# Kernel tuning notes

Measured on AMD Instinct MI355X. Metric: run time of the kernel, lower is better.

The kernel has to match this reference:

```python
import jax, jax.numpy as jnp
import numpy as np

N_CLASS, N_SUPPORT, N_QUERY = 5, 5, 15
C, T, V = 128, 8, 25
LN_EPS = 1e-12


def setup_inputs() -> dict:
    key = jax.random.key(0)
    ks = jax.random.split(key, 6)
    n_tot = N_CLASS * (N_SUPPORT + N_QUERY)
    inp = jax.random.normal(ks[0], (n_tot, C, T, V), dtype=jnp.float32)
    # episode labels: 20 consecutive samples per class (arange // per_class)
    target = (jnp.arange(n_tot, dtype=jnp.int32) // (N_SUPPORT + N_QUERY)).astype(jnp.int32)
    s = 0.02
    p = lambda k: jax.random.normal(k, (C, C), dtype=jnp.float32) * s
    return {
        'input': inp,
        'Wq': p(ks[1]), 'bq': jnp.zeros((C,), jnp.float32),
        'Wk': p(ks[2]), 'bk': jnp.zeros((C,), jnp.float32),
        'Wv': p(ks[3]), 'bv': jnp.zeros((C,), jnp.float32),
        'Wo': p(ks[4]), 'bo': jnp.zeros((C,), jnp.float32),
        'ln_g': jnp.ones((C,), jnp.float32), 'ln_b': jnp.zeros((C,), jnp.float32),
        'target': target,
        'n_support': N_SUPPORT,
    }


def _layer_norm(x, g, b):
    mu = x.mean(-1, keepdims=True)
    var = ((x - mu) ** 2).mean(-1, keepdims=True)
    return (x - mu) * jax.lax.rsqrt(var + LN_EPS) * g + b


def _episode_forward(input, Wq, bq, Wk, bk, Wv, bv, Wo, bo, ln_g, ln_b, target, n_support):
    n_tot, c, t, v = input.shape
    m = N_CLASS
    per_class = n_tot // m
    n_query = per_class - n_support
    n = m * n_query

    # support/query split (stable argsort == torch.where per class for sorted labels)
    order = jnp.argsort(target).reshape(m, per_class)
    supp_idx = order[:, :n_support]                      # (m, h)
    qry_idx = order[:, n_support:].reshape(-1)           # (n,)
    z_proto = input[supp_idx]                            # (m, h, c, t, v)
    zq = input[qry_idx]                                  # (n, c, t, v)

    # ---- hal(): pairwise cross-attention over the vertex axis ----
    mh = m * n_support
    zq_p = jnp.transpose(zq, (0, 2, 3, 1))                                   # (n, t, v, c)
    zp_p = jnp.transpose(z_proto.reshape(mh, c, t, v), (0, 2, 3, 1))          # (mh, t, v, c)
    cat = jnp.concatenate([zq_p, zp_p], axis=0)                               # (n1, t, v, c)
    n1 = cat.shape[0]

    # Q from each of the n1 items, K/V from each of the mh prototypes.
    # Equivalent to the original expand->reshape pairing, without duplicating K/V.
    Q = cat @ Wq + bq                                                         # (n1, t, v, c)
    K = zp_p @ Wk + bk                                                        # (mh, t, v, c)
    Vv = zp_p @ Wv + bv                                                       # (mh, t, v, c)
    scale = 1.0 / jnp.sqrt(jnp.asarray(c, dtype=Q.dtype))
    scores = jnp.einsum('ntqc,mtkc->nmtqk', Q, K) * scale                     # (n1, mh, t, v, v)
    attn = jax.nn.softmax(scores, axis=-1)
    ctx = jnp.einsum('nmtqk,mtkc->nmtqc', attn, Vv)                           # (n1, mh, t, v, c)
    out = _layer_norm(ctx @ Wo + bo + cat[:, None], ln_g, ln_b)               # residual + LN
    att = out.mean(axis=1)                                                    # (n1, t, v, c) mean over mh pairs

    zq_att = jnp.transpose(att[:n], (0, 3, 1, 2))                             # (n, c, t, v)
    proto_att = att[n:].reshape(m, n_support, t, v, c).mean(axis=1)           # (m, t, v, c)
    proto_att = jnp.transpose(proto_att, (0, 3, 1, 2))                        # (m, c, t, v)

    # ---- squared-Euclidean metric on flattened features ----
    zq_f = zq_att.reshape(n, -1)
    zp_f = proto_att.reshape(m, -1)
    dist = jnp.sum((zq_f[:, None, :] - zp_f[None, :, :]) ** 2, axis=-1)       # (n, m)

    log_p_y = jax.nn.log_softmax(-dist, axis=1).reshape(m, n_query, m)
    cls = jnp.arange(m)
    loss = -log_p_y[cls[:, None], jnp.arange(n_query)[None, :], cls[:, None]].mean()
    y_hat = jnp.argmax(log_p_y, axis=2)
    acc = (y_hat == cls[:, None]).astype(jnp.float32).mean()
    return loss, acc


def reference(input, Wq, bq, Wk, bk, Wv, bv, Wo, bo, ln_g, ln_b, target, n_support):
    return _episode_forward(input, Wq, bq, Wk, bk, Wv, bv, Wo, bo, ln_g, ln_b, target, n_support)
```

## Files before the change

kernel.cpp:

```cpp
#include <hip/hip_runtime.h>
#include <math.h>

#define NTOT 100
#define NQ   75
#define NP   25
#define CC   128
#define TT   8
#define VV   25
#define NCLS 5
#define NSUP 5
#define NQRY 15
#define ROW  (TT*VV*CC)
#define TILE (VV*CC)
#define ROWS_Q 20000
#define ROWS_S 5000
#define RB_Q 625
#define RB_S 157

typedef __attribute__((ext_vector_type(8))) short short8;
typedef __attribute__((ext_vector_type(16))) float f32x16;

typedef union { uint4 u4; short8 s8; } pk_t;

__device__ __forceinline__ ushort f2bf(float f) {
    uint u = __float_as_uint(f);
    u += 0x7FFFu + ((u >> 16) & 1u);
    return (ushort)(u >> 16);
}
__device__ __forceinline__ float bf2f(uint u16v) {
    return __uint_as_float(u16v << 16);
}
__device__ __forceinline__ uint pkbf(float a, float b) {
    return (uint)f2bf(a) | ((uint)f2bf(b) << 16);
}

__global__ __launch_bounds__(256) void k_pack(
    const float* __restrict__ Wq, const float* __restrict__ Wk,
    const float* __restrict__ Wv, const float* __restrict__ Wo,
    ushort* __restrict__ WfG) {
    int which = blockIdx.x;
    const float* W = (which == 0) ? Wq : (which == 1) ? Wk : (which == 2) ? Wv : Wo;
    ushort* dstbase = WfG + (size_t)which * 16384;
    for (int o = threadIdx.x; o < 2048; o += 256) {
        int k8 = o >> 7, c = o & 127;
        uint4 pk;
        pk.x = pkbf(W[(k8*8+0)*128 + c], W[(k8*8+1)*128 + c]);
        pk.y = pkbf(W[(k8*8+2)*128 + c], W[(k8*8+3)*128 + c]);
        pk.z = pkbf(W[(k8*8+4)*128 + c], W[(k8*8+5)*128 + c]);
        pk.w = pkbf(W[(k8*8+6)*128 + c], W[(k8*8+7)*128 + c]);
        int dst = (((c >> 5) * 8 + (k8 >> 1)) * 64 + ((c & 31) + 32 * (k8 & 1))) * 8;
        *(uint4*)(dstbase + dst) = pk;
    }
}

__global__ __launch_bounds__(256) void k_proj(
    const float* __restrict__ input, const int* __restrict__ target,
    const ushort* __restrict__ WfG,
    const float* __restrict__ bq, const float* __restrict__ bk,
    const float* __restrict__ bv,
    ushort* __restrict__ catC, ushort* __restrict__ Qf,
    ushort* __restrict__ Kf, ushort* __restrict__ Vf,
    int* __restrict__ counter) {
    __shared__ ushort stage[32 * 132];
    __shared__ ushort VtF[4096];
    __shared__ int iscr[200];

    int bid = blockIdx.x, tid = threadIdx.x;
    int w = tid >> 6, lane = tid & 63, half = lane >> 5, l31 = lane & 31;

    if (bid == 0 && tid == 0) *counter = 0;

    if (tid < NTOT) iscr[tid] = target[tid];
    __syncthreads();
    if (tid < NTOT) {
        int ti = iscr[tid], rank = 0;
        for (int j = 0; j < NTOT; ++j) {
            int tj = iscr[j];
            rank += (tj < ti) || (tj == ti && j < tid);
        }
        iscr[100 + rank] = tid;
    }
    __syncthreads();

    bool isQ = bid >= RB_S;
    int rowblk = isQ ? bid - RB_S : bid;
    int rlimit = isQ ? ROWS_Q : ROWS_S;
    int g0 = rowblk * 32;
    int gend = min(g0 + 32, rlimit);

    for (int nn = g0 / 200; nn <= (gend - 1) / 200; ++nn) {
        int lo = max(g0 - nn * 200, 0);
        int hi = min(gend - 1 - nn * 200, 199);
        int len = hi - lo + 1;
        int nidx = isQ ? nn : (NQ + nn);
        int src;
        if (nidx < NQ) { int m = nidx / NQRY, qq = nidx - m * NQRY; src = iscr[100 + m * 20 + NSUP + qq]; }
        else           { int i2 = nidx - NQ; int m = i2 / NSUP, s = i2 - m * NSUP; src = iscr[100 + m * 20 + s]; }
        const float* inb = input + (size_t)src * ROW + lo;
        int rbase = nn * 200 + lo - g0;
        for (int idx = tid; idx < len * 128; idx += 256) {
            int c = idx / len, k = idx - c * len;
            stage[(rbase + k) * 132 + c] = f2bf(inb[c * 200 + k]);
        }
    }
    __syncthreads();

    short8 af[8];
    #pragma unroll
    for (int ks = 0; ks < 8; ++ks)
        af[ks] = *(const short8*)&stage[l31 * 132 + ks * 16 + half * 8];

    #define CHAIN(A, OUT, BASE) do {                                             \
        const ushort* bp_ = (BASE) + w * 4096 + lane * 8;                        \
        _Pragma("unroll")                                                        \
        for (int ks = 0; ks < 8; ++ks) {                                         \
            short8 bf_ = *(const short8*)(bp_ + ks * 512);                       \
            OUT = __builtin_amdgcn_mfma_f32_32x32x16_bf16(A[ks], bf_, OUT, 0, 0, 0); \
        }                                                                        \
    } while (0)

    if (isQ) {
        f32x16 Cm;
        #pragma unroll
        for (int r = 0; r < 16; ++r) Cm[r] = 0.f;
        CHAIN(af, Cm, WfG);
        float bcol = bq[w * 32 + l31];
        int c = w * 32 + l31;
        #pragma unroll
        for (int r = 0; r < 16; ++r) {
            int row = g0 + (r & 3) + 8 * (r >> 2) + 4 * half;
            int st = row / 25, vv = row - st * 25;
            size_t dst = (((size_t)st * 8 + (c >> 4)) * 64 + (vv + 32 * ((c >> 3) & 1))) * 8 + (c & 7);
            Qf[dst] = f2bf(Cm[r] + bcol);
        }
        uint* cc = (uint*)catC + (size_t)g0 * 64;
        for (int idx = tid; idx < 2048; idx += 256) {
            int row = idx >> 6, c2 = (idx & 63) * 2;
            cc[idx] = (uint)stage[row * 132 + c2] | ((uint)stage[row * 132 + c2 + 1] << 16);
        }
    } else {
        {
            f32x16 Cm;
            #pragma unroll
            for (int r = 0; r < 16; ++r) Cm[r] = 0.f;
            CHAIN(af, Cm, WfG + 16384);
            float bcol = bk[w * 32 + l31];
            int c = w * 32 + l31;
            #pragma unroll
            for (int r = 0; r < 16; ++r) {
                int row = g0 + (r & 3) + 8 * (r >> 2) + 4 * half;
                if (row < ROWS_S) {
                    int st = row / 25, vv = row - st * 25;
                    size_t dst = (((size_t)st * 8 + (c >> 4)) * 64 + (vv + 32 * ((c >> 3) & 1))) * 8 + (c & 7);
                    Kf[dst] = f2bf(Cm[r] + bcol);
                }
            }
        }
        {
            f32x16 Cm;
            #pragma unroll
            for (int r = 0; r < 16; ++r) Cm[r] = 0.f;
            CHAIN(af, Cm, WfG + 32768);
            float bcol = bv[w * 32 + l31];
            int c = w * 32 + l31;
            int ks2 = c >> 4, kh = (c >> 3) & 1, j2 = c & 7;
            #pragma unroll
            for (int r = 0; r < 16; ++r) {
                int rowLocal = (r & 3) + 8 * (r >> 2) + 4 * half;
                VtF[ks2 * 512 + (rowLocal + 32 * kh) * 8 + j2] = f2bf(Cm[r] + bcol);
            }
        }
        __syncthreads();
        short8 a2[8];
        #pragma unroll
        for (int ks = 0; ks < 8; ++ks)
            a2[ks] = *(const short8*)&VtF[ks * 512 + lane * 8];
        {
            f32x16 Cm;
            #pragma unroll
            for (int r = 0; r < 16; ++r) Cm[r] = 0.f;
            CHAIN(a2, Cm, WfG + 49152);
            int c = w * 32 + l31;
            #pragma unroll
            for (int r = 0; r < 16; ++r) {
                int row = g0 + (r & 3) + 8 * (r >> 2) + 4 * half;
                if (row < ROWS_S) {
                    int tile = row / 25, vv = row - tile * 25;
                    size_t dst = ((((size_t)tile * 4 + (c >> 5)) * 2 + (vv >> 4)) * 64
                                  + ((c & 31) + 32 * ((vv & 15) >> 3))) * 8 + (vv & 7);
                    Vf[dst] = f2bf(Cm[r]);
                }
            }
        }
    }
    #undef CHAIN
}

__global__ __launch_bounds__(256, 2) void k_attn(
    const ushort* __restrict__ Qf, const ushort* __restrict__ Kf,
    const ushort* __restrict__ Vf, const ushort* __restrict__ catC,
    const float* __restrict__ bo, float* __restrict__ att) {
    __shared__ __align__(16) char smem[26016];
    float*  catb = (float*)smem;
    ushort* qls  = (ushort*)(smem + 12912);
    float (*red)[50][65] = (float (*)[50][65])smem;

    int pair = blockIdx.x;
    int t = pair & 7;
    int tid = threadIdx.x;
    int wv = tid >> 6, lane = tid & 63;
    int q = lane & 31, half = lane >> 5;

    {
        const uint* cc = (const uint*)catC + (size_t)pair * 1600;
        for (int i2 = tid; i2 < 1600; i2 += 256) {
            uint u = cc[i2];
            int r = i2 >> 6, c2 = (i2 & 63) * 2;
            catb[r * 129 + c2]     = bf2f(u & 0xffffu) + bo[c2];
            catb[r * 129 + c2 + 1] = bf2f(u >> 16) + bo[c2 + 1];
        }
    }
    {
        const uint* qp = (const uint*)(Qf + (size_t)pair * 4096);
        uint* ql = (uint*)qls;
        for (int i2 = tid; i2 < 2048; i2 += 256) ql[i2] = qp[i2];
    }
    __syncthreads();

    int qc = q < 25 ? q : 24;
    float attsum[64];
    #pragma unroll
    for (int i = 0; i < 64; ++i) attsum[i] = 0.f;
    float Csc = 0.f;

    const float CEXP = (float)(1.4426950408889634 * 0.08838834764831845);

    const ushort* kbase = Kf + (size_t)t * 4096 + lane * 8;
    short8 kf[8];
    #pragma unroll
    for (int ks = 0; ks < 8; ++ks)
        kf[ks] = *(const short8*)(kbase + (size_t)wv * 32768 + ks * 512);

    int cnt = (wv == 0) ? 7 : 6;
    for (int mi = 0; mi < cnt; ++mi) {
        int m = wv + 4 * mi;

        f32x16 S;
        #pragma unroll
        for (int r = 0; r < 16; ++r) S[r] = 0.f;
        #pragma unroll
        for (int ks = 0; ks < 8; ++ks) {
            short8 qv = *(const short8*)(qls + ks * 512 + lane * 8);
            S = __builtin_amdgcn_mfma_f32_32x32x16_bf16(kf[ks], qv, S, 0, 0, 0);
        }

        float p[16], mx = -3e38f;
        #pragma unroll
        for (int r = 0; r < 16; ++r) {
            int key = (r & 3) + 8 * (r >> 2) + 4 * half;
            float v = (key < 25) ? S[r] : -3e38f;
            p[r] = v; mx = fmaxf(mx, v);
        }
        mx = fmaxf(mx, __shfl_xor(mx, 32));
        float sum = 0.f;
        #pragma unroll
        for (int r = 0; r < 16; ++r) { p[r] = exp2f((p[r] - mx) * CEXP); sum += p[r]; }
        sum += __shfl_xor(sum, 32);
        float inv = 1.f / sum;

        const ushort* vp = Vf + ((size_t)(m * 8 + t)) * 4096 + lane * 8;
        short8 vf0 = *(const short8*)(vp);
        short8 vf1 = *(const short8*)(vp + 512);
        short8 vf2 = *(const short8*)(vp + 1024);
        short8 vf3 = *(const short8*)(vp + 1536);
        short8 vf4 = *(const short8*)(vp + 2048);
        short8 vf5 = *(const short8*)(vp + 2560);
        short8 vf6 = *(const short8*)(vp + 3072);
        short8 vf7 = *(const short8*)(vp + 3584);
        #pragma unroll
        for (int ks = 0; ks < 8; ++ks)
            kf[ks] = *(const short8*)(kbase + (size_t)(m + 4) * 32768 + ks * 512);

        uint o01   = pkbf(p[0] * inv,  p[1] * inv);
        uint o23   = pkbf(p[2] * inv,  p[3] * inv);
        uint o45   = pkbf(p[4] * inv,  p[5] * inv);
        uint o67   = pkbf(p[6] * inv,  p[7] * inv);
        uint o89   = pkbf(p[8] * inv,  p[9] * inv);
        uint o1011 = pkbf(p[10] * inv, p[11] * inv);
        uint o1213 = pkbf(p[12] * inv, p[13] * inv);
        uint o1415 = pkbf(p[14] * inv, p[15] * inv);
        bool h0 = (half == 0);
        uint rA = __shfl_xor(h0 ? o45 : o01, 32);
        uint rB = __shfl_xor(h0 ? o67 : o23, 32);
        uint rC = __shfl_xor(h0 ? o1213 : o89, 32);
        uint rD = __shfl_xor(h0 ? o1415 : o1011, 32);
        pk_t P0, P1;
        P0.u4 = h0 ? make_uint4(o01, o23, rA, rB) : make_uint4(rA, rB, o45, o67);
        P1.u4 = h0 ? make_uint4(o89, o1011, rC, rD) : make_uint4(rC, rD, o1213, o1415);
        short8 pb0 = P0.s8, pb1 = P1.s8;

        f32x16 ctx[4];
        #pragma unroll
        for (int mt = 0; mt < 4; ++mt) {
            #pragma unroll
            for (int r = 0; r < 16; ++r) ctx[mt][r] = 0.f;
        }
        ctx[0] = __builtin_amdgcn_mfma_f32_32x32x16_bf16(vf0, pb0, ctx[0], 0, 0, 0);
        ctx[0] = __builtin_amdgcn_mfma_f32_32x32x16_bf16(vf1, pb1, ctx[0], 0, 0, 0);
        ctx[1] = __builtin_amdgcn_mfma_f32_32x32x16_bf16(vf2, pb0, ctx[1], 0, 0, 0);
        ctx[1] = __builtin_amdgcn_mfma_f32_32x32x16_bf16(vf3, pb1, ctx[1], 0, 0, 0);
        ctx[2] = __builtin_amdgcn_mfma_f32_32x32x16_bf16(vf4, pb0, ctx[2], 0, 0, 0);
        ctx[2] = __builtin_amdgcn_mfma_f32_32x32x16_bf16(vf5, pb1, ctx[2], 0, 0, 0);
        ctx[3] = __builtin_amdgcn_mfma_f32_32x32x16_bf16(vf6, pb0, ctx[3], 0, 0, 0);
        ctx[3] = __builtin_amdgcn_mfma_f32_32x32x16_bf16(vf7, pb1, ctx[3], 0, 0, 0);

        float s1 = 0.f, s2 = 0.f;
        #pragma unroll
        for (int mt = 0; mt < 4; ++mt) {
            float t1 = 0.f, t2 = 0.f;
            #pragma unroll
            for (int r = 0; r < 16; ++r) {
                int c = mt * 32 + (r & 3) + 8 * (r >> 2) + 4 * half;
                float xv = ctx[mt][r] + catb[qc * 129 + c];
                ctx[mt][r] = xv;
                t1 += xv; t2 = fmaf(xv, xv, t2);
            }
            s1 += t1; s2 += t2;
        }
        s1 += __shfl_xor(s1, 32); s2 += __shfl_xor(s2, 32);
        float mu = s1 * (1.f / 128.f);
        float var = s2 * (1.f / 128.f) - mu * mu;
        var = fmaxf(var, 0.f);
        float rs = rsqrtf(var + 1e-12f);
        #pragma unroll
        for (int i = 0; i < 64; ++i)
            attsum[i] = fmaf(ctx[i >> 4][i & 15], rs, attsum[i]);
        Csc = fmaf(-mu, rs, Csc);
    }

    __syncthreads();
    int s = half * 25 + q;
    bool act = q < 25;
    if ((wv == 1 || wv == 3) && act) {
        float (*rg)[65] = red[wv >> 1];
        #pragma unroll
        for (int i = 0; i < 64; ++i) rg[s][i] = attsum[i];
        rg[s][64] = Csc;
    }
    __syncthreads();
    if ((wv == 0 || wv == 2) && act) {
        float (*rg)[65] = red[wv >> 1];
        #pragma unroll
        for (int i = 0; i < 64; ++i) attsum[i] += rg[s][i];
        Csc += rg[s][64];
    }
    __syncthreads();
    if (wv == 2 && act) {
        #pragma unroll
        for (int i = 0; i < 64; ++i) red[0][s][i] = attsum[i];
        red[0][s][64] = Csc;
    }
    __syncthreads();
    if (wv == 0 && act) {
        #pragma unroll
        for (int i = 0; i < 64; ++i) attsum[i] += red[0][s][i];
        Csc += red[0][s][64];
        float* ap = att + (size_t)pair * TILE + q * 128;
        #pragma unroll
        for (int mt = 0; mt < 4; ++mt) {
            #pragma unroll
            for (int rg4 = 0; rg4 < 4; ++rg4) {
                int c0 = mt * 32 + 8 * rg4 + 4 * half;
                int i0 = mt * 16 + rg4 * 4;
                float4 o;
                o.x = attsum[i0 + 0] + Csc; o.y = attsum[i0 + 1] + Csc;
                o.z = attsum[i0 + 2] + Csc; o.w = attsum[i0 + 3] + Csc;
                *(float4*)&ap[c0] = o;
            }
        }
    }
}

__global__ __launch_bounds__(256) void k_proto(
    const float* __restrict__ att, float* __restrict__ proto) {
    int b = blockIdx.x;
    int j = b >> 3, chunk = b & 7;
    const float4* s0 = (const float4*)(att + (size_t)(NQ + j * 5 + 0) * ROW);
    const float4* s1 = (const float4*)(att + (size_t)(NQ + j * 5 + 1) * ROW);
    const float4* s2 = (const float4*)(att + (size_t)(NQ + j * 5 + 2) * ROW);
    const float4* s3 = (const float4*)(att + (size_t)(NQ + j * 5 + 3) * ROW);
    const float4* s4 = (const float4*)(att + (size_t)(NQ + j * 5 + 4) * ROW);
    float4* pr = (float4*)(proto + (size_t)j * ROW);
    int e0 = chunk * 800, e1 = e0 + 800;
    for (int e4 = e0 + threadIdx.x; e4 < e1; e4 += 256) {
        float4 q0 = s0[e4], q1 = s1[e4], q2 = s2[e4], q3 = s3[e4], q4 = s4[e4];
        float4 o;
        o.x = 0.2f * (q0.x + q1.x + q2.x + q3.x + q4.x);
        o.y = 0.2f * (q0.y + q1.y + q2.y + q3.y + q4.y);
        o.z = 0.2f * (q0.z + q1.z + q2.z + q3.z + q4.z);
        o.w = 0.2f * (q0.w + q1.w + q2.w + q3.w + q4.w);
        pr[e4] = o;
    }
}

__global__ __launch_bounds__(256) void k_dist_loss(
    const float* __restrict__ att, const float* __restrict__ proto,
    const float* __restrict__ ln_g,
    float* __restrict__ dist, int* __restrict__ counter,
    float* __restrict__ out) {
    int b = blockIdx.x;
    int i = b / 5, j = b - 5 * i;
    const float4* a = (const float4*)(att + (size_t)i * ROW);
    const float4* p = (const float4*)(proto + (size_t)j * ROW);
    float d = 0.f;
    for (int e4 = threadIdx.x; e4 < 6400; e4 += 256) {
        float4 av = a[e4];
        float4 pv = p[e4];
        float4 g4 = *(const float4*)(ln_g + (e4 & 31) * 4);
        float dx = av.x - pv.x, dy = av.y - pv.y, dz = av.z - pv.z, dw = av.w - pv.w;
        d = fmaf(g4.x * g4.x, dx * dx, d);
        d = fmaf(g4.y * g4.y, dy * dy, d);
        d = fmaf(g4.z * g4.z, dz * dz, d);
        d = fmaf(g4.w * g4.w, dw * dw, d);
    }
    #pragma unroll
    for (int msk = 32; msk >= 1; msk >>= 1) d += __shfl_xor(d, msk);
    __shared__ float part[4];
    __shared__ int lastFlag;
    int lane = threadIdx.x & 63, wv = threadIdx.x >> 6;
    if (lane == 0) part[wv] = d;
    __syncthreads();
    if (threadIdx.x == 0) {
        float total = (part[0] + part[1] + part[2] + part[3]) * (1.f / 625.f);
        __hip_atomic_store(&dist[b], total, __ATOMIC_RELEASE, __HIP_MEMORY_SCOPE_AGENT);
        int tk = __hip_atomic_fetch_add(counter, 1, __ATOMIC_ACQ_REL, __HIP_MEMORY_SCOPE_AGENT);
        lastFlag = (tk == 374);
    }
    __syncthreads();
    if (!lastFlag) return;

    int iq = threadIdx.x;
    float li = 0.f, ok = 0.f;
    if (iq < NQ) {
        float dd[5];
        #pragma unroll
        for (int jj = 0; jj < 5; ++jj)
            dd[jj] = __hip_atomic_load(&dist[iq * 5 + jj], __ATOMIC_ACQUIRE, __HIP_MEMORY_SCOPE_AGENT);
        int cls = iq / NQRY;
        float mind = dd[0];
        int best = 0;
        #pragma unroll
        for (int jj = 1; jj < 5; ++jj) {
            if (dd[jj] < mind) mind = dd[jj];
            if (dd[jj] < dd[best]) best = jj;
        }
        float sume = 0.f;
        #pragma unroll
        for (int jj = 0; jj < 5; ++jj) sume += expf(mind - dd[jj]);
        float lse = logf(sume) - mind;
        li = dd[cls] + lse;
        ok = (best == cls) ? 1.f : 0.f;
    }
    #pragma unroll
    for (int msk = 32; msk >= 1; msk >>= 1) {
        li += __shfl_xor(li, msk);
        ok += __shfl_xor(ok, msk);
    }
    if (lane == 0) { part[wv] = li; part[wv + 2] = ok; }
    __syncthreads();
    if (threadIdx.x == 0) {
        out[0] = (part[0] + part[1]) / 75.f;
        out[1] = (part[2] + part[3]) / 75.f;
    }
}

extern "C" void kernel_launch(void* const* d_in, const int* in_sizes, int n_in,
                              void* d_out, int out_size, void* d_ws, size_t ws_size,
                              hipStream_t stream) {
    const float* input = (const float*)d_in[0];
    const float* Wq   = (const float*)d_in[1];
    const float* bq   = (const float*)d_in[2];
    const float* Wk   = (const float*)d_in[3];
    const float* bk   = (const float*)d_in[4];
    const float* Wv   = (const float*)d_in[5];
    const float* bv   = (const float*)d_in[6];
    const float* Wo   = (const float*)d_in[7];
    const float* bo   = (const float*)d_in[8];
    const float* ln_g = (const float*)d_in[9];
    const float* ln_b = (const float*)d_in[10];
    const int* target = (const int*)d_in[11];
    float* out = (float*)d_out;
    (void)ln_b;

    float* ws = (float*)d_ws;
    ushort* catC = (ushort*)ws;
    ushort* Qf   = catC + 2560000;
    ushort* Kf   = Qf + 3276800;
    ushort* Vf   = Kf + 819200;
    float*  att  = (float*)(Vf + 819200);
    float*  distb = att + 2560000;
    int*    counter = (int*)(distb + 512);
    ushort* WfG  = (ushort*)(counter + 16);
    float*  proto = (float*)catC;

    k_pack<<<4, 256, 0, stream>>>(Wq, Wk, Wv, Wo, WfG);
    k_proj<<<RB_Q + RB_S, 256, 0, stream>>>(input, target, WfG, bq, bk, bv,
                                            catC, Qf, Kf, Vf, counter);
    k_attn<<<800, 256, 0, stream>>>(Qf, Kf, Vf, catC, bo, att);
    k_proto<<<40, 256, 0, stream>>>(att, proto);
    k_dist_loss<<<375, 256, 0, stream>>>(att, proto, ln_g, distb, counter, out);
}
```

Before: 176.0 us.

## Enlarge projection row blocks, vectorize staging loads, fuse prototype mean into distance

The projection kernel now handles 128 rows per block instead of 32, looping over 32-row MFMA groups. This cuts the block count and amortizes the per-block argsort rank computation. Staging loads use float4 reads when the segment is aligned, with a scalar fallback otherwise. The separate prototype-averaging kernel is removed and its 5-way mean is recomputed inside the distance kernel, saving one launch and the proto buffer round trip at the cost of 5x more support reads per distance block. The larger row blocks also use more shared memory and leave fewer blocks to fill the GPU.

New measurement: 184.2 us. 4.6% more time.

```diff
diff --git a/kernel.cpp b/kernel.cpp
--- a/kernel.cpp
+++ b/kernel.cpp
@@ -14,8 +14,8 @@
 #define TILE (VV*CC)
 #define ROWS_Q 20000
 #define ROWS_S 5000
-#define RB_Q 625
-#define RB_S 157
+#define NB_KV 40
+#define NB_Q  157
 
 typedef __attribute__((ext_vector_type(8))) short short8;
 typedef __attribute__((ext_vector_type(16))) float f32x16;
@@ -61,7 +61,7 @@
     ushort* __restrict__ catC, ushort* __restrict__ Qf,
     ushort* __restrict__ Kf, ushort* __restrict__ Vf,
     int* __restrict__ counter) {
-    __shared__ ushort stage[32 * 132];
+    __shared__ ushort stage[128 * 132];
     __shared__ ushort VtF[4096];
     __shared__ int iscr[200];
 
@@ -82,11 +82,11 @@
     }
     __syncthreads();
 
-    bool isQ = bid >= RB_S;
-    int rowblk = isQ ? bid - RB_S : bid;
+    bool isQ = bid >= NB_KV;
+    int rowblk = isQ ? bid - NB_KV : bid;
     int rlimit = isQ ? ROWS_Q : ROWS_S;
-    int g0 = rowblk * 32;
-    int gend = min(g0 + 32, rlimit);
+    int g0 = rowblk * 128;
+    int gend = min(g0 + 128, rlimit);
 
     for (int nn = g0 / 200; nn <= (gend - 1) / 200; ++nn) {
         int lo = max(g0 - nn * 200, 0);
@@ -98,17 +98,31 @@
         else           { int i2 = nidx - NQ; int m = i2 / NSUP, s = i2 - m * NSUP; src = iscr[100 + m * 20 + s]; }
         const float* inb = input + (size_t)src * ROW + lo;
         int rbase = nn * 200 + lo - g0;
-        for (int idx = tid; idx < len * 128; idx += 256) {
-            int c = idx / len, k = idx - c * len;
-            stage[(rbase + k) * 132 + c] = f2bf(inb[c * 200 + k]);
-        }
-    }
-    __syncthreads();
-
-    short8 af[8];
-    #pragma unroll
-    for (int ks = 0; ks < 8; ++ks)
-        af[ks] = *(const short8*)&stage[l31 * 132 + ks * 16 + half * 8];
+        if (((lo & 3) == 0) && ((len & 3) == 0)) {
+            int nv4 = len >> 2;
+            int total4 = nv4 << 7;
+            int qstep = 256 / nv4, rstep = 256 - qstep * nv4;
+            int c = tid / nv4, v = tid - c * nv4;
+            for (int idx = tid; idx < total4; idx += 256) {
+                int k = v << 2;
+                float4 f = *(const float4*)(inb + c * 200 + k);
+                int ro = (rbase + k) * 132 + c;
+                stage[ro]       = f2bf(f.x);
+                stage[ro + 132] = f2bf(f.y);
+                stage[ro + 264] = f2bf(f.z);
+                stage[ro + 396] = f2bf(f.w);
+                c += qstep; v += rstep;
+                if (v >= nv4) { v -= nv4; ++c; }
+            }
+        } else {
+            int total = len * 128;
+            for (int idx = tid; idx < total; idx += 256) {
+                int c = idx / len, k = idx - c * len;
+                stage[(rbase + k) * 132 + c] = f2bf(inb[c * 200 + k]);
+            }
+        }
+    }
+    __syncthreads();
 
     #define CHAIN(A, OUT, BASE) do {                                             \
         const ushort* bp_ = (BASE) + w * 4096 + lane * 8;                        \
@@ -119,78 +133,96 @@
         }                                                                        \
     } while (0)
 
+    int ngrp = (gend - g0 + 31) >> 5;
+
     if (isQ) {
-        f32x16 Cm;
-        #pragma unroll
-        for (int r = 0; r < 16; ++r) Cm[r] = 0.f;
-        CHAIN(af, Cm, WfG);
-        float bcol = bq[w * 32 + l31];
-        int c = w * 32 + l31;
-        #pragma unroll
-        for (int r = 0; r < 16; ++r) {
-            int row = g0 + (r & 3) + 8 * (r >> 2) + 4 * half;
-            int st = row / 25, vv = row - st * 25;
-            size_t dst = (((size_t)st * 8 + (c >> 4)) * 64 + (vv + 32 * ((c >> 3) & 1))) * 8 + (c & 7);
-            Qf[dst] = f2bf(Cm[r] + bcol);
+        for (int rg = 0; rg < ngrp; ++rg) {
+            int lrow0 = rg * 32;
+            short8 af[8];
+            #pragma unroll
+            for (int ks = 0; ks < 8; ++ks)
+                af[ks] = *(const short8*)&stage[(lrow0 + l31) * 132 + ks * 16 + half * 8];
+            f32x16 Cm;
+            #pragma unroll
+            for (int r = 0; r < 16; ++r) Cm[r] = 0.f;
+            CHAIN(af, Cm, WfG);
+            float bcol = bq[w * 32 + l31];
+            int c = w * 32 + l31;
+            #pragma unroll
+            for (int r = 0; r < 16; ++r) {
+                int row = g0 + lrow0 + (r & 3) + 8 * (r >> 2) + 4 * half;
+                int st = row / 25, vv = row - st * 25;
+                size_t dst = (((size_t)st * 8 + (c >> 4)) * 64 + (vv + 32 * ((c >> 3) & 1))) * 8 + (c & 7);
+                Qf[dst] = f2bf(Cm[r] + bcol);
+            }
         }
         uint* cc = (uint*)catC + (size_t)g0 * 64;
-        for (int idx = tid; idx < 2048; idx += 256) {
+        int ncc = (gend - g0) * 64;
+        for (int idx = tid; idx < ncc; idx += 256) {
             int row = idx >> 6, c2 = (idx & 63) * 2;
             cc[idx] = (uint)stage[row * 132 + c2] | ((uint)stage[row * 132 + c2 + 1] << 16);
         }
     } else {
-        {
-            f32x16 Cm;
-            #pragma unroll
-            for (int r = 0; r < 16; ++r) Cm[r] = 0.f;
-            CHAIN(af, Cm, WfG + 16384);
-            float bcol = bk[w * 32 + l31];
-            int c = w * 32 + l31;
-            #pragma unroll
-            for (int r = 0; r < 16; ++r) {
-                int row = g0 + (r & 3) + 8 * (r >> 2) + 4 * half;
-                if (row < ROWS_S) {
-                    int st = row / 25, vv = row - st * 25;
-                    size_t dst = (((size_t)st * 8 + (c >> 4)) * 64 + (vv + 32 * ((c >> 3) & 1))) * 8 + (c & 7);
-                    Kf[dst] = f2bf(Cm[r] + bcol);
+        for (int rg = 0; rg < ngrp; ++rg) {
+            int lrow0 = rg * 32;
+            short8 af[8];
+            #pragma unroll
+            for (int ks = 0; ks < 8; ++ks)
+                af[ks] = *(const short8*)&stage[(lrow0 + l31) * 132 + ks * 16 + half * 8];
+            {
+                f32x16 Cm;
+                #pragma unroll
+                for (int r = 0; r < 16; ++r) Cm[r] = 0.f;
+                CHAIN(af, Cm, WfG + 16384);
+                float bcol = bk[w * 32 + l31];
+                int c = w * 32 + l31;
+                #pragma unroll
+                for (int r = 0; r < 16; ++r) {
+                    int row = g0 + lrow0 + (r & 3) + 8 * (r >> 2) + 4 * half;
+                    if (row < ROWS_S) {
+                        int st = row / 25, vv = row - st * 25;
+                        size_t dst = (((size_t)st * 8 + (c >> 4)) * 64 + (vv + 32 * ((c >> 3) & 1))) * 8 + (c & 7);
+                        Kf[dst] = f2bf(Cm[r] + bcol);
+                    }
                 }
             }
-        }
-        {
-            f32x16 Cm;
-            #pragma unroll
-            for (int r = 0; r < 16; ++r) Cm[r] = 0.f;
-            CHAIN(af, Cm, WfG + 32768);
-            float bcol = bv[w * 32 + l31];
-            int c = w * 32 + l31;
-            int ks2 = c >> 4, kh = (c >> 3) & 1, j2 = c & 7;
-            #pragma unroll
-            for (int r = 0; r < 16; ++r) {
-                int rowLocal = (r & 3) + 8 * (r >> 2) + 4 * half;
-                VtF[ks2 * 512 + (rowLocal + 32 * kh) * 8 + j2] = f2bf(Cm[r] + bcol);
-            }
-        }
-        __syncthreads();
-        short8 a2[8];
-        #pragma unroll
-        for (int ks = 0; ks < 8; ++ks)
-            a2[ks] = *(const short8*)&VtF[ks * 512 + lane * 8];
-        {
-            f32x16 Cm;
-            #pragma unroll
-            for (int r = 0; r < 16; ++r) Cm[r] = 0.f;
-            CHAIN(a2, Cm, WfG + 49152);
-            int c = w * 32 + l31;
-            #pragma unroll
-            for (int r = 0; r < 16; ++r) {
-                int row = g0 + (r & 3) + 8 * (r >> 2) + 4 * half;
-                if (row < ROWS_S) {
-                    int tile = row / 25, vv = row - tile * 25;
-                    size_t dst = ((((size_t)tile * 4 + (c >> 5)) * 2 + (vv >> 4)) * 64
-                                  + ((c & 31) + 32 * ((vv & 15) >> 3))) * 8 + (vv & 7);
-                    Vf[dst] = f2bf(Cm[r]);
+            {
+                f32x16 Cm;
+                #pragma unroll
+                for (int r = 0; r < 16; ++r) Cm[r] = 0.f;
+                CHAIN(af, Cm, WfG + 32768);
+                float bcol = bv[w * 32 + l31];
+                int c = w * 32 + l31;
+                int ks2 = c >> 4, kh = (c >> 3) & 1, j2 = c & 7;
+                #pragma unroll
+                for (int r = 0; r < 16; ++r) {
+                    int rowLocal = (r & 3) + 8 * (r >> 2) + 4 * half;
+                    VtF[ks2 * 512 + (rowLocal + 32 * kh) * 8 + j2] = f2bf(Cm[r] + bcol);
                 }
             }
+            __syncthreads();
+            short8 a2[8];
+            #pragma unroll
+            for (int ks = 0; ks < 8; ++ks)
+                a2[ks] = *(const short8*)&VtF[ks * 512 + lane * 8];
+            {
+                f32x16 Cm;
+                #pragma unroll
+                for (int r = 0; r < 16; ++r) Cm[r] = 0.f;
+                CHAIN(a2, Cm, WfG + 49152);
+                int c = w * 32 + l31;
+                #pragma unroll
+                for (int r = 0; r < 16; ++r) {
+                    int row = g0 + lrow0 + (r & 3) + 8 * (r >> 2) + 4 * half;
+                    if (row < ROWS_S) {
+                        int tile = row / 25, vv = row - tile * 25;
+                        size_t dst = ((((size_t)tile * 4 + (c >> 5)) * 2 + (vv >> 4)) * 64
+                                      + ((c & 31) + 32 * ((vv & 15) >> 3))) * 8 + (vv & 7);
+                        Vf[dst] = f2bf(Cm[r]);
+                    }
+                }
+            }
+            __syncthreads();
         }
     }
     #undef CHAIN
@@ -381,43 +413,28 @@
     }
 }
 
-__global__ __launch_bounds__(256) void k_proto(
-    const float* __restrict__ att, float* __restrict__ proto) {
-    int b = blockIdx.x;
-    int j = b >> 3, chunk = b & 7;
-    const float4* s0 = (const float4*)(att + (size_t)(NQ + j * 5 + 0) * ROW);
-    const float4* s1 = (const float4*)(att + (size_t)(NQ + j * 5 + 1) * ROW);
-    const float4* s2 = (const float4*)(att + (size_t)(NQ + j * 5 + 2) * ROW);
-    const float4* s3 = (const float4*)(att + (size_t)(NQ + j * 5 + 3) * ROW);
-    const float4* s4 = (const float4*)(att + (size_t)(NQ + j * 5 + 4) * ROW);
-    float4* pr = (float4*)(proto + (size_t)j * ROW);
-    int e0 = chunk * 800, e1 = e0 + 800;
-    for (int e4 = e0 + threadIdx.x; e4 < e1; e4 += 256) {
-        float4 q0 = s0[e4], q1 = s1[e4], q2 = s2[e4], q3 = s3[e4], q4 = s4[e4];
-        float4 o;
-        o.x = 0.2f * (q0.x + q1.x + q2.x + q3.x + q4.x);
-        o.y = 0.2f * (q0.y + q1.y + q2.y + q3.y + q4.y);
-        o.z = 0.2f * (q0.z + q1.z + q2.z + q3.z + q4.z);
-        o.w = 0.2f * (q0.w + q1.w + q2.w + q3.w + q4.w);
-        pr[e4] = o;
-    }
-}
-
 __global__ __launch_bounds__(256) void k_dist_loss(
-    const float* __restrict__ att, const float* __restrict__ proto,
-    const float* __restrict__ ln_g,
+    const float* __restrict__ att, const float* __restrict__ ln_g,
     float* __restrict__ dist, int* __restrict__ counter,
     float* __restrict__ out) {
     int b = blockIdx.x;
     int i = b / 5, j = b - 5 * i;
-    const float4* a = (const float4*)(att + (size_t)i * ROW);
-    const float4* p = (const float4*)(proto + (size_t)j * ROW);
+    const float4* a  = (const float4*)(att + (size_t)i * ROW);
+    const float4* s0 = (const float4*)(att + (size_t)(NQ + j * 5 + 0) * ROW);
+    const float4* s1p = (const float4*)(att + (size_t)(NQ + j * 5 + 1) * ROW);
+    const float4* s2p = (const float4*)(att + (size_t)(NQ + j * 5 + 2) * ROW);
+    const float4* s3p = (const float4*)(att + (size_t)(NQ + j * 5 + 3) * ROW);
+    const float4* s4p = (const float4*)(att + (size_t)(NQ + j * 5 + 4) * ROW);
     float d = 0.f;
     for (int e4 = threadIdx.x; e4 < 6400; e4 += 256) {
         float4 av = a[e4];
-        float4 pv = p[e4];
+        float4 q0 = s0[e4], q1 = s1p[e4], q2 = s2p[e4], q3 = s3p[e4], q4 = s4p[e4];
         float4 g4 = *(const float4*)(ln_g + (e4 & 31) * 4);
-        float dx = av.x - pv.x, dy = av.y - pv.y, dz = av.z - pv.z, dw = av.w - pv.w;
+        float px = 0.2f * (q0.x + q1.x + q2.x + q3.x + q4.x);
+        float py = 0.2f * (q0.y + q1.y + q2.y + q3.y + q4.y);
+        float pz = 0.2f * (q0.z + q1.z + q2.z + q3.z + q4.z);
+        float pw = 0.2f * (q0.w + q1.w + q2.w + q3.w + q4.w);
+        float dx = av.x - px, dy = av.y - py, dz = av.z - pz, dw = av.w - pw;
         d = fmaf(g4.x * g4.x, dx * dx, d);
         d = fmaf(g4.y * g4.y, dy * dy, d);
         d = fmaf(g4.z * g4.z, dz * dz, d);
@@ -501,12 +518,10 @@
     float*  distb = att + 2560000;
     int*    counter = (int*)(distb + 512);
     ushort* WfG  = (ushort*)(counter + 16);
-    float*  proto = (float*)catC;
 
     k_pack<<<4, 256, 0, stream>>>(Wq, Wk, Wv, Wo, WfG);
-    k_proj<<<RB_Q + RB_S, 256, 0, stream>>>(input, target, WfG, bq, bk, bv,
-                                            catC, Qf, Kf, Vf, counter);
+    k_proj<<<NB_KV + NB_Q, 256, 0, stream>>>(input, target, WfG, bq, bk, bv,
+                                             catC, Qf, Kf, Vf, counter);
     k_attn<<<800, 256, 0, stream>>>(Qf, Kf, Vf, catC, bo, att);
-    k_proto<<<40, 256, 0, stream>>>(att, proto);
-    k_dist_loss<<<375, 256, 0, stream>>>(att, proto, ln_g, distb, counter, out);
-}
+    k_dist_loss<<<375, 256, 0, stream>>>(att, ln_g, distb, counter, out);
+}
```
